# Kernel optimization log

Measured on AMD Instinct MI355X. Metric: run time of the kernel, lower is better.

## Reference

```python
import jax, jax.numpy as jnp
import numpy as np

N, C, H, W = 2, 32, 56, 56   # batch, in_channels, spatial
O = 64                        # out_channels
PAD = 1                       # ConstantPad2d padding


def _shift(a, dh, dw):
    """Zero-padded shift: out[..., i, j] = a[..., i+dh, j+dw] (out of range -> 0)."""
    nd = a.ndim
    if dh:
        a = jnp.pad(a[..., dh:, :], [(0, 0)] * (nd - 2) + [(0, dh), (0, 0)])
    if dw:
        a = jnp.pad(a[..., :, dw:], [(0, 0)] * (nd - 2) + [(0, 0), (0, dw)])
    return a


def setup_inputs() -> dict:
    key = jax.random.key(0)
    k1, k2, k3 = jax.random.split(key, 3)
    x = jax.random.normal(k1, (N, C, H, W), dtype=jnp.float32)
    # weight entries are used as divisors in extract_param_p; keep them bounded
    # away from zero (magnitude in [0.5, 1.5], random sign) for a stable baseline.
    mag = jax.random.uniform(k2, (O, C, 3, 3), minval=0.5, maxval=1.5, dtype=jnp.float32)
    sgn = jnp.where(jax.random.bernoulli(k3, 0.5, (O, C, 3, 3)), 1.0, -1.0).astype(jnp.float32)
    return {"x": x, "weight": mag * sgn}


def reference(x, weight):
    w = weight  # [O, C, 3, 3]
    # --- extract predict filter P = [p0, p1, p2, p3], each [O, C] ---
    p0 = -w[:, :, 2, 0] / w[:, :, 2, 1]
    p1 = -w[:, :, 0, 2] / w[:, :, 1, 2]
    p2 = (1.0 - w[:, :, 0, 0]
          + w[:, :, 2, 0] * w[:, :, 0, 1] / w[:, :, 2, 1]
          + w[:, :, 0, 2] * w[:, :, 1, 0] / w[:, :, 1, 2]) / w[:, :, 1, 1]
    p3 = -w[:, :, 2, 2] / w[:, :, 1, 1]
    # --- extract update filter U = [u0..u4], each [O, C] ---
    u0, u1, u2, u3, u4 = (w[:, :, 0, 1], w[:, :, 2, 1],
                          w[:, :, 1, 0], w[:, :, 1, 2], w[:, :, 1, 1])

    def bc(c):  # [O, C] -> broadcastable over [N, O, C, Hp, Wp]
        return c[None, :, :, None, None]

    # forward: ConstantPad2d then vanilla lifting scheme (aux_index = 2).
    xp = jnp.pad(x, ((0, 0), (0, 0), (PAD, PAD), (PAD, PAD)))  # [N, C, Hp, Wp]
    x5 = xp[:, None, :, :, :]                                  # [N, 1, C, Hp, Wp]

    x0 = x5
    x1 = _shift(x5, 0, 1)
    x2 = _shift(x5, 1, 0)
    x3 = _shift(x5, 1, 1)
    x0_2 = _shift(x5, 2, 2)

    # predict steps (broadcast to [N, O, C, Hp, Wp])
    x1 = x1 - bc(p0) * x0
    x2 = x2 - bc(p1) * x0
    x3 = x3 - bc(p2) * x0 - bc(p3) * x0_2

    x1_2 = _shift(x1, 2, 0)
    x2_2 = _shift(x2, 0, 2)

    # update steps
    out = (x0
           + bc(u0) * x1 + bc(u1) * x1_2
           + bc(u2) * x2 + bc(u3) * x2_2
           + bc(u4) * x3)

    # crop aux_index=2 border, then sum over in_channels (channel_split loop
    # processes contiguous O slices and concatenates -> identical to full O).
    return out[:, :, :, :-2, :-2].sum(axis=2)  # [N, O, H, W]
```

## Files before the change

### kernel.cpp

```cpp
#include <hip/hip_runtime.h>


namespace {
constexpr int Cc = 32, Hh = 56, Ww = 56, Oo = 64;

__global__ __launch_bounds__(256)
void lifting_conv_kernel(const float* __restrict__ x,
                         const float* __restrict__ w,
                         float* __restrict__ out)
{
    __shared__ float xs[Cc * 4 * 60];

    const int tid = threadIdx.x;
    const int og  = blockIdx.x;
    const int ip  = blockIdx.y;
    const int n   = blockIdx.z;
    const int i0  = ip * 2;

    for (int e = tid; e < Cc * 4 * 58; e += 256) {
        const int c   = e / (4 * 58);
        const int rem = e - c * (4 * 58);
        const int r   = rem / 58;
        const int jj  = rem - r * 58;
        const int h   = i0 - 1 + r;
        const int col = jj - 1;
        float v = 0.0f;
        if ((unsigned)h < (unsigned)Hh && (unsigned)col < (unsigned)Ww)
            v = x[((n * Cc + c) * Hh + h) * Ww + col];
        xs[(c * 4 + r) * 60 + jj] = v;
    }
    __syncthreads();

    const int lane = tid & 63;
    const int wv   = tid >> 6;
    if (lane >= 56) return;
    const int rsub = (lane >= 28) ? 1 : 0;
    const int cp   = lane - rsub * 28;
    const int col0 = cp * 2;

    const int o_base = __builtin_amdgcn_readfirstlane(og * 16 + wv * 4);
    const float* __restrict__ wb = w + (size_t)o_base * Cc * 9;

    float acc[4][2];
    #pragma unroll
    for (int i = 0; i < 4; ++i) { acc[i][0] = 0.f; acc[i][1] = 0.f; }

    const float* xbase = &xs[rsub * 60 + col0];

    #pragma unroll 2
    for (int c = 0; c < Cc; ++c) {
        const float* xr = xbase + c * 240;
        const float2 r0a = *(const float2*)(xr);
        const float2 r0b = *(const float2*)(xr + 2);
        const float2 r1a = *(const float2*)(xr + 60);
        const float2 r1b = *(const float2*)(xr + 62);
        const float2 r2a = *(const float2*)(xr + 120);
        const float2 r2b = *(const float2*)(xr + 122);

        #pragma unroll
        for (int oo = 0; oo < 4; ++oo) {
            const float* wc = wb + (oo * Cc + c) * 9;
            const float w0 = wc[0], w1 = wc[1], w2 = wc[2],
                        w3 = wc[3], w4 = wc[4], w5 = wc[5],
                        w6 = wc[6], w7 = wc[7], w8 = wc[8];
            acc[oo][0] += w0 * r0a.x + w1 * r0a.y + w2 * r0b.x
                        + w3 * r1a.x + w4 * r1a.y + w5 * r1b.x
                        + w6 * r2a.x + w7 * r2a.y + w8 * r2b.x;
            acc[oo][1] += w0 * r0a.y + w1 * r0b.x + w2 * r0b.y
                        + w3 * r1a.y + w4 * r1b.x + w5 * r1b.y
                        + w6 * r2a.y + w7 * r2b.x + w8 * r2b.y;
        }
    }

    const int row = i0 + rsub;
    #pragma unroll
    for (int oo = 0; oo < 4; ++oo) {
        float2 v; v.x = acc[oo][0]; v.y = acc[oo][1];
        *(float2*)(out + ((size_t)(n * Oo + o_base + oo) * Hh + row) * Ww + col0) = v;
    }
}
}

extern "C" void kernel_launch(void* const* d_in, const int* in_sizes, int n_in,
                              void* d_out, int out_size, void* d_ws, size_t ws_size,
                              hipStream_t stream)
{
    const float* x = (const float*)d_in[0];
    const float* w = (const float*)d_in[1];
    float* out = (float*)d_out;

    dim3 grid(4, 28, 2);
    lifting_conv_kernel<<<grid, 256, 0, stream>>>(x, w, out);
}
```

Baseline: 73.99 us.

## Split input channels across four wave groups and reduce partials in LDS

Blocks grow from 256 to 1024 threads. Each group of four waves handles 8 of the 32 input channels for the same output tile, and the partial sums are reduced through shared memory before the store. This cuts the serial channel loop per wave and raises occupancy on a small grid of 224 blocks. In exchange it adds two barriers and an LDS reduction, and reuses the input tile buffer for the partials.

```diff
diff --git a/kernel.cpp b/kernel.cpp
--- a/kernel.cpp
+++ b/kernel.cpp
@@ -4,7 +4,10 @@
 namespace {
 constexpr int Cc = 32, Hh = 56, Ww = 56, Oo = 64;
 
-__global__ __launch_bounds__(256)
+constexpr int RSTRIDE = 10;
+constexpr int REGION  = 576;
+
+__global__ __launch_bounds__(1024, 4)
 void lifting_conv_kernel(const float* __restrict__ x,
                          const float* __restrict__ w,
                          float* __restrict__ out)
@@ -17,7 +20,7 @@
     const int n   = blockIdx.z;
     const int i0  = ip * 2;
 
-    for (int e = tid; e < Cc * 4 * 58; e += 256) {
+    for (int e = tid; e < Cc * 4 * 58; e += 1024) {
         const int c   = e / (4 * 58);
         const int rem = e - c * (4 * 58);
         const int r   = rem / 58;
@@ -33,23 +36,27 @@
 
     const int lane = tid & 63;
     const int wv   = tid >> 6;
-    if (lane >= 56) return;
-    const int rsub = (lane >= 28) ? 1 : 0;
-    const int cp   = lane - rsub * 28;
+    const int oq   = wv & 3;
+    const int cch  = wv >> 2;
+    const bool act = lane < 56;
+    const int lact = act ? lane : 0;
+    const int rsub = (lact >= 28) ? 1 : 0;
+    const int cp   = lact - rsub * 28;
     const int col0 = cp * 2;
 
-    const int o_base = __builtin_amdgcn_readfirstlane(og * 16 + wv * 4);
-    const float* __restrict__ wb = w + (size_t)o_base * Cc * 9;
+    const int o_base = __builtin_amdgcn_readfirstlane(og * 16 + oq * 4);
+    const int cbeg   = __builtin_amdgcn_readfirstlane(cch * 8);
+    const float* __restrict__ wb = w + ((size_t)o_base * Cc + cbeg) * 9;
 
     float acc[4][2];
     #pragma unroll
     for (int i = 0; i < 4; ++i) { acc[i][0] = 0.f; acc[i][1] = 0.f; }
 
-    const float* xbase = &xs[rsub * 60 + col0];
+    const float* xbase = &xs[cbeg * 240 + rsub * 60 + col0];
 
     #pragma unroll 2
-    for (int c = 0; c < Cc; ++c) {
-        const float* xr = xbase + c * 240;
+    for (int cc = 0; cc < 8; ++cc) {
+        const float* xr = xbase + cc * 240;
         const float2 r0a = *(const float2*)(xr);
         const float2 r0b = *(const float2*)(xr + 2);
         const float2 r1a = *(const float2*)(xr + 60);
@@ -59,7 +66,7 @@
 
         #pragma unroll
         for (int oo = 0; oo < 4; ++oo) {
-            const float* wc = wb + (oo * Cc + c) * 9;
+            const float* wc = wb + (oo * Cc + cc) * 9;
             const float w0 = wc[0], w1 = wc[1], w2 = wc[2],
                         w3 = wc[3], w4 = wc[4], w5 = wc[5],
                         w6 = wc[6], w7 = wc[7], w8 = wc[8];
@@ -72,11 +79,33 @@
         }
     }
 
-    const int row = i0 + rsub;
-    #pragma unroll
-    for (int oo = 0; oo < 4; ++oo) {
-        float2 v; v.x = acc[oo][0]; v.y = acc[oo][1];
-        *(float2*)(out + ((size_t)(n * Oo + o_base + oo) * Hh + row) * Ww + col0) = v;
+    __syncthreads();
+
+    if (cch > 0 && act) {
+        float* p = &xs[((cch - 1) * 4 + oq) * REGION + lane * RSTRIDE];
+        #pragma unroll
+        for (int oo = 0; oo < 4; ++oo)
+            *(float2*)(p + oo * 2) = make_float2(acc[oo][0], acc[oo][1]);
+    }
+    __syncthreads();
+
+    if (cch == 0 && act) {
+        #pragma unroll
+        for (int pi = 0; pi < 3; ++pi) {
+            const float* p = &xs[(pi * 4 + oq) * REGION + lane * RSTRIDE];
+            #pragma unroll
+            for (int oo = 0; oo < 4; ++oo) {
+                const float2 v = *(const float2*)(p + oo * 2);
+                acc[oo][0] += v.x;
+                acc[oo][1] += v.y;
+            }
+        }
+        const int row = i0 + rsub;
+        #pragma unroll
+        for (int oo = 0; oo < 4; ++oo) {
+            float2 v; v.x = acc[oo][0]; v.y = acc[oo][1];
+            *(float2*)(out + ((size_t)(n * Oo + o_base + oo) * Hh + row) * Ww + col0) = v;
+        }
     }
 }
 }
@@ -90,5 +119,5 @@
     float* out = (float*)d_out;
 
     dim3 grid(4, 28, 2);
-    lifting_conv_kernel<<<grid, 256, 0, stream>>>(x, w, out);
+    lifting_conv_kernel<<<grid, 1024, 0, stream>>>(x, w, out);
 }
```

Result: faster. 62.43 us (-15.6%).
